# Performance work log

Hardware: AMD Instinct MI355X
Metric: run time of the kernel (lower is better)

Reference implementation:

```python
import jax, jax.numpy as jnp
import numpy as np

B, M, D = 16, 16, 512          # m (tokens per sample) must equal num_experts
N = 16                          # num_experts
H = (D + D) * 2 // 3            # hidden_dim = 682
OUT = 512


def setup_inputs() -> dict:
    key = jax.random.key(0)
    ks = jax.random.split(key, 8)
    s = lambda k, shape, fan: jax.random.normal(k, shape, jnp.float32) / np.sqrt(fan)
    return {
        "x":    jax.random.normal(ks[0], (B, M, D), jnp.float32),
        "phi":  jax.random.normal(ks[1], (D, N, H), jnp.float32),
        "W1":   s(ks[2], (N, D, H), D),
        "b1":   s(ks[3], (N, H), D),
        "W2":   s(ks[4], (N, H, D), H),
        "b2":   s(ks[5], (N, D), H),
        "Wout": s(ks[6], (N * D, OUT), N * D),
        "bout": s(ks[7], (OUT,), N * D),
    }


def reference(x, phi, W1, b1, W2, b2, Wout, bout):
    # dispatch/combine logits: [b, m, n, p]
    logits = jnp.einsum('bmd,dnp->bmnp', x, phi)
    Dw = jax.nn.softmax(logits, axis=1)                       # dispatch weights over tokens m
    Cw = jax.nn.softmax(jax.nn.softmax(logits, axis=2), axis=3)  # (softmax of softmax, faithful)
    Xs = jnp.einsum('bmd,bmnp->bnpd', x, Dw)                  # expert slot inputs [b,n,p,d]
    # batched per-expert MLP (grouped GEMM over expert axis n)
    hmid = jax.nn.relu(jnp.einsum('bnpd,ndh->bnph', Xs, W1) + b1[None, :, None, :])
    Ys = jnp.einsum('bnph,nhd->bnpd', hmid, W2) + b2[None, :, None, :]
    Y = jnp.einsum('bnpd,bmnp->bmd', Ys, Cw)                  # combine -> [b, m, d]
    flat = Y.reshape(Y.shape[0], -1)                          # [b, m*d] == [b, n*d]
    return flat @ Wout + bout
```

## Files before the change

kernel.cpp:

```cpp
#include <hip/hip_runtime.h>
#include <hip/hip_bf16.h>
#include <math.h>

typedef unsigned int   u32;
typedef unsigned short u16;
typedef __bf16 bf16;
typedef bf16  bf16x8  __attribute__((ext_vector_type(8)));
typedef float f32x4   __attribute__((ext_vector_type(4)));
typedef float f32x16  __attribute__((ext_vector_type(16)));

#define BBATCH 16
#define MTOK   16
#define NEXP   16
#define DDIM   512
#define HDIM   682
#define HPAD   704
#define NHCOL  (NEXP*HDIM)
#define NHPCOL (NEXP*HPAD)

__device__ __forceinline__ u16 f2bf(float f) {
    u32 u = __builtin_bit_cast(u32, f);
    u += 0x7fffu + ((u >> 16) & 1u);
    return (u16)(u >> 16);
}
__device__ __forceinline__ float bf2f(u16 h) {
    u32 u = ((u32)h) << 16;
    return __builtin_bit_cast(float, u);
}
__device__ __forceinline__ u32 pk2bf(float a, float b) {
    __hip_bfloat162 t = __float22bfloat162_rn(float2{a, b});
    u32 r;
    __builtin_memcpy(&r, &t, 4);
    return r;
}

__global__ __launch_bounds__(256) void k_prep(
    const float* __restrict__ x, const float* __restrict__ b2,
    const float* __restrict__ bout,
    u16* __restrict__ xh, u16* __restrict__ xl,
    float* __restrict__ Y, float* __restrict__ out, u16* __restrict__ DwT) {
    const int bid = blockIdx.x, tid = threadIdx.x;
    if (bid < 128) {
        int i = (bid * 256 + tid) * 4;
        float4 v = *(const float4*)&x[i];
        float a[4] = {v.x, v.y, v.z, v.w};
        u16 hh[4], ll[4];
        #pragma unroll
        for (int j = 0; j < 4; ++j) {
            hh[j] = f2bf(a[j]);
            ll[j] = f2bf(a[j] - bf2f(hh[j]));
        }
        *(uint2*)&xh[i] = make_uint2((u32)hh[0] | ((u32)hh[1] << 16), (u32)hh[2] | ((u32)hh[3] << 16));
        *(uint2*)&xl[i] = make_uint2((u32)ll[0] | ((u32)ll[1] << 16), (u32)ll[2] | ((u32)ll[3] << 16));
    } else if (bid < 640) {
        int idx = (bid - 128) * 256 + tid;
        int d = idx & 511;
        float s = 0.f;
        #pragma unroll
        for (int nn = 0; nn < 16; ++nn) s += b2[nn * 512 + d];
        Y[idx] = s;
    } else if (bid < 672) {
        int idx = (bid - 640) * 256 + tid;
        out[idx] = bout[idx & 511];
    } else {
        int g = (bid - 672) * 256 + tid;
        int bn = g / 88, off = g - bn * 88;
        *(uint2*)(DwT + (size_t)(bn * HPAD + HDIM) * 16 + off * 4) = make_uint2(0u, 0u);
    }
}

__global__ __launch_bounds__(256) void k_lt1(
    const u16* __restrict__ xh, const u16* __restrict__ xl,
    const float* __restrict__ phi, const float* __restrict__ W1,
    float* __restrict__ logits, u16* __restrict__ DwT, u16* __restrict__ T1b) {
    __shared__ __align__(16) char SMEM[29184];
    const int bid = blockIdx.x, tid = threadIdx.x;
    const int wv = tid >> 6, lane = tid & 63, quad = lane >> 4, l15 = lane & 15;
    if (bid < 684) {
        const int ct = bid % 171, rt = bid / 171;
        u16* AH = (u16*)SMEM;
        u16* AL = (u16*)(SMEM + 5120);
        u16* BH = (u16*)(SMEM + 10240);
        u16* BL = (u16*)(SMEM + 15360);
        float* F = (float*)(SMEM + 20480);
        f32x4 acc[4] = {};
        for (int kb = 0; kb < 512; kb += 32) {
            {
                int r = tid >> 2, kg = (tid & 3) * 8;
                size_t ao = (size_t)(rt * 64 + r) * 512 + kb + kg;
                *(uint4*)&AH[r * 40 + kg] = *(const uint4*)(xh + ao);
                *(uint4*)&AL[r * 40 + kg] = *(const uint4*)(xl + ao);
            }
            {
                int dl = tid >> 3, cg = (tid & 7) * 8;
                int c0 = ct * 64 + cg;
                const float* src = phi + (size_t)(kb + dl) * NHCOL + c0;
                float v[8];
                if (c0 + 8 <= NHCOL) {
                    *(float4*)&v[0] = *(const float4*)&src[0];
                    *(float4*)&v[4] = *(const float4*)&src[4];
                } else {
                    #pragma unroll
                    for (int i = 0; i < 8; ++i) v[i] = (c0 + i < NHCOL) ? src[i] : 0.f;
                }
                #pragma unroll
                for (int i = 0; i < 8; ++i) F[dl * 68 + cg + i] = v[i];
            }
            __syncthreads();
            {
                int cc = tid & 63, q = tid >> 6;
                u16 th[8], tl[8];
                #pragma unroll
                for (int i = 0; i < 8; ++i) {
                    float v = F[(q * 8 + i) * 68 + cc];
                    th[i] = f2bf(v);
                    tl[i] = f2bf(v - bf2f(th[i]));
                }
                *(uint4*)&BH[cc * 40 + q * 8] = *(uint4*)&th[0];
                *(uint4*)&BL[cc * 40 + q * 8] = *(uint4*)&tl[0];
            }
            __syncthreads();
            bf16x8 ah = *(const bf16x8*)&AH[(wv * 16 + l15) * 40 + quad * 8];
            bf16x8 al = *(const bf16x8*)&AL[(wv * 16 + l15) * 40 + quad * 8];
            #pragma unroll
            for (int j = 0; j < 4; ++j) {
                bf16x8 bh = *(const bf16x8*)&BH[(j * 16 + l15) * 40 + quad * 8];
                bf16x8 bl = *(const bf16x8*)&BL[(j * 16 + l15) * 40 + quad * 8];
                acc[j] = __builtin_amdgcn_mfma_f32_16x16x32_bf16(ah, bh, acc[j], 0, 0, 0);
                acc[j] = __builtin_amdgcn_mfma_f32_16x16x32_bf16(ah, bl, acc[j], 0, 0, 0);
                acc[j] = __builtin_amdgcn_mfma_f32_16x16x32_bf16(al, bh, acc[j], 0, 0, 0);
            }
            __syncthreads();
        }
        const int b  = rt * 4 + wv;
        const int r0 = rt * 64 + wv * 16 + quad * 4;
        #pragma unroll
        for (int j = 0; j < 4; ++j) {
            const int col = ct * 64 + j * 16 + l15;
            float a0 = acc[j][0], a1 = acc[j][1], a2 = acc[j][2], a3 = acc[j][3];
            if (col < NHCOL) {
                logits[(size_t)(r0 + 0) * NHCOL + col] = a0;
                logits[(size_t)(r0 + 1) * NHCOL + col] = a1;
                logits[(size_t)(r0 + 2) * NHCOL + col] = a2;
                logits[(size_t)(r0 + 3) * NHCOL + col] = a3;
            }
            float mx = fmaxf(fmaxf(a0, a1), fmaxf(a2, a3));
            mx = fmaxf(mx, __shfl_xor(mx, 16));
            mx = fmaxf(mx, __shfl_xor(mx, 32));
            float e0 = expf(a0 - mx), e1 = expf(a1 - mx);
            float e2 = expf(a2 - mx), e3 = expf(a3 - mx);
            float s = e0 + e1 + e2 + e3;
            s += __shfl_xor(s, 16);
            s += __shfl_xor(s, 32);
            float inv = 1.f / s;
            if (col < NHCOL) {
                int n = col / HDIM;
                int p = col - n * HDIM;
                u16* dst = DwT + ((size_t)((b * 16 + n) * HPAD + p)) * 16 + quad * 4;
                *(uint2*)dst = make_uint2(pk2bf(e0 * inv, e1 * inv), pk2bf(e2 * inv, e3 * inv));
            }
        }
    } else {
        const int w = bid - 684;
        const int ct = w >> 1, rh = w & 1;
        const int n = ct / 11, h0 = (ct % 11) * 64;
        u16* As = (u16*)SMEM;
        u16* Bs = (u16*)(SMEM + 10240);
        float* F = (float*)(SMEM + 15360);
        f32x4 acc[2][4] = {};
        for (int kb = 0; kb < 512; kb += 32) {
            {
                int r = tid >> 1, kg = (tid & 1) * 16;
                const u16* s = xh + (size_t)(rh * 128 + r) * 512 + kb + kg;
                *(uint4*)&As[r * 40 + kg]     = *(const uint4*)s;
                *(uint4*)&As[r * 40 + kg + 8] = *(const uint4*)(s + 8);
            }
            {
                int dl = tid >> 3, cg = (tid & 7) * 8;
                int h = h0 + cg;
                const float* wr = W1 + ((size_t)n * 512 + kb + dl) * HDIM + h;
                float v[8];
                if (h + 8 <= HDIM) {
                    #pragma unroll
                    for (int i = 0; i < 4; ++i) {
                        float2 t = *(const float2*)&wr[i * 2];
                        v[i * 2] = t.x; v[i * 2 + 1] = t.y;
                    }
                } else {
                    #pragma unroll
                    for (int i = 0; i < 8; ++i) v[i] = (h + i < HDIM) ? wr[i] : 0.f;
                }
                #pragma unroll
                for (int i = 0; i < 8; ++i) F[dl * 68 + cg + i] = v[i];
            }
            __syncthreads();
            {
                int cc = tid & 63, q = tid >> 6;
                u16 tv[8];
                #pragma unroll
                for (int i = 0; i < 8; ++i) tv[i] = f2bf(F[(q * 8 + i) * 68 + cc]);
                *(uint4*)&Bs[cc * 40 + q * 8] = *(uint4*)&tv[0];
            }
            __syncthreads();
            bf16x8 af[2], bfr[4];
            #pragma unroll
            for (int i = 0; i < 2; ++i)
                af[i] = *(const bf16x8*)&As[(wv * 32 + i * 16 + l15) * 40 + quad * 8];
            #pragma unroll
            for (int j = 0; j < 4; ++j)
                bfr[j] = *(const bf16x8*)&Bs[(j * 16 + l15) * 40 + quad * 8];
            #pragma unroll
            for (int i = 0; i < 2; ++i)
                #pragma unroll
                for (int j = 0; j < 4; ++j)
                    acc[i][j] = __builtin_amdgcn_mfma_f32_16x16x32_bf16(af[i], bfr[j], acc[i][j], 0, 0, 0);
            __syncthreads();
        }
        #pragma unroll
        for (int i = 0; i < 2; ++i)
            #pragma unroll
            for (int j = 0; j < 4; ++j) {
                int col = ct * 64 + j * 16 + l15;
                int r0  = rh * 128 + wv * 32 + i * 16 + quad * 4;
                #pragma unroll
                for (int r = 0; r < 4; ++r)
                    T1b[(size_t)(r0 + r) * NHPCOL + col] = f2bf(acc[i][j][r]);
            }
    }
}

__global__ __launch_bounds__(256) void k_cw(
    const float* __restrict__ L, u16* __restrict__ CwB) {
    __shared__ float row[NHCOL];
    const int bid = blockIdx.x, tid = threadIdx.x;
    const int m = bid & 15, b = bid >> 4;
    const float* Lrow = L + (size_t)(b * 16 + m) * NHCOL;
    for (int i = tid; i < NHCOL; i += 256) row[i] = Lrow[i];
    __syncthreads();
    for (int p = tid; p < HDIM; p += 256) {
        float v[16];
        float mx = -1e30f;
        #pragma unroll
        for (int n = 0; n < 16; ++n) { v[n] = row[n * HDIM + p]; mx = fmaxf(mx, v[n]); }
        float s = 0.f;
        #pragma unroll
        for (int n = 0; n < 16; ++n) { v[n] = expf(v[n] - mx); s += v[n]; }
        float inv = 1.f / s;
        #pragma unroll
        for (int n = 0; n < 16; ++n) row[n * HDIM + p] = expf(v[n] * inv);
    }
    __syncthreads();
    const int wv = tid >> 6, lane = tid & 63;
    for (int nn = 0; nn < 4; ++nn) {
        int n = wv * 4 + nn;
        float s = 0.f;
        for (int p = lane; p < HDIM; p += 64) s += row[n * HDIM + p];
        #pragma unroll
        for (int off = 32; off > 0; off >>= 1) s += __shfl_xor(s, off);
        float inv = 1.f / s;
        u16* dst = CwB + (size_t)(((b * 16 + n) * 16 + m)) * HPAD;
        for (int p = lane; p < HDIM; p += 64) dst[p] = f2bf(row[n * HDIM + p] * inv);
        if (lane < HPAD - HDIM) dst[HDIM + lane] = 0;
    }
}

__global__ __launch_bounds__(256) void k_mid(
    const u16* __restrict__ T1b, const u16* __restrict__ DwT,
    const u16* __restrict__ CwB, const float* __restrict__ b1,
    u16* __restrict__ Gb) {
    __shared__ u16 T1T[128 * 24];
    __shared__ u16 hmidT[128 * 64];
    const int ht = blockIdx.x, n = blockIdx.y, b = blockIdx.z;
    const int tid = threadIdx.x;
    const int wv = tid >> 6, lane = tid & 63;
    const int quad = lane >> 4, l15 = lane & 15;
    const int l31 = lane & 31, half = lane >> 5;
    const int h0 = ht * 128;
    const int b16n = b * 16 + n;

    {
        int m = tid & 15, hh0 = (tid >> 4) * 8;
        u16 v[8];
        if (h0 + hh0 + 8 <= HPAD) {
            *(uint4*)v = *(const uint4*)(T1b + (size_t)(b * 16 + m) * NHPCOL + n * HPAD + h0 + hh0);
        } else {
            #pragma unroll
            for (int i = 0; i < 8; ++i) v[i] = 0;
        }
        #pragma unroll
        for (int i = 0; i < 8; ++i) T1T[(hh0 + i) * 24 + m] = v[i];
    }
    __syncthreads();

    const int hrow = wv * 32 + l31;
    bf16x8 bt1 = *(const bf16x8*)&T1T[hrow * 24 + half * 8];
    int hg1 = h0 + hrow;
    float biasf = (hg1 < HDIM) ? b1[n * HDIM + hg1] : 0.f;
    f32x16 cbias;
    #pragma unroll
    for (int i = 0; i < 16; ++i) cbias[i] = biasf;

    const u16* dwbase = DwT + (size_t)(b16n * HPAD) * 16;
    const u16* cwrow  = CwB + (size_t)(b16n * 16 + l15) * HPAD;

    f32x4 acc[2] = {};
    const int hsw = hrow & 7;
    for (int c = 0; c < 11; ++c) {
        const int p0 = c * 64;
        #pragma unroll
        for (int pt = 0; pt < 2; ++pt) {
            bf16x8 adw = *(const bf16x8*)(dwbase + (size_t)(p0 + pt * 32 + l31) * 16 + half * 8);
            f32x16 hm = __builtin_amdgcn_mfma_f32_32x32x16_bf16(adw, bt1, cbias, 0, 0, 0);
            #pragma unroll
            for (int g = 0; g < 4; ++g) {
                float v0 = fmaxf(hm[g * 4 + 0], 0.f);
                float v1 = fmaxf(hm[g * 4 + 1], 0.f);
                float v2 = fmaxf(hm[g * 4 + 2], 0.f);
                float v3 = fmaxf(hm[g * 4 + 3], 0.f);
                uint2 pk = make_uint2(pk2bf(v0, v1), pk2bf(v2, v3));
                int gran = (pt * 4 + g) ^ hsw;
                *(uint2*)&hmidT[hrow * 64 + gran * 8 + half * 4] = pk;
            }
        }
        #pragma unroll
        for (int s = 0; s < 2; ++s) {
            bf16x8 acw = *(const bf16x8*)(cwrow + p0 + s * 32 + quad * 8);
            #pragma unroll
            for (int hj = 0; hj < 2; ++hj) {
                int hr = wv * 32 + hj * 16 + l15;
                int gr = (s * 4 + quad) ^ (hr & 7);
                bf16x8 bh = *(const bf16x8*)&hmidT[hr * 64 + gr * 8];
                acc[hj] = __builtin_amdgcn_mfma_f32_16x16x32_bf16(acw, bh, acc[hj], 0, 0, 0);
            }
        }
    }
    #pragma unroll
    for (int hj = 0; hj < 2; ++hj) {
        int h = h0 + wv * 32 + hj * 16 + l15;
        if (h < HPAD) {
            #pragma unroll
            for (int r = 0; r < 4; ++r) {
                int m = quad * 4 + r;
                Gb[(size_t)(b * 16 + m) * NHPCOL + n * HPAD + h] = f2bf(acc[hj][r]);
            }
        }
    }
}

__global__ __launch_bounds__(256) void k_ygemm(
    const u16* __restrict__ G, const float* __restrict__ W2, float* __restrict__ Y) {
    __shared__ u16 AsL[64 * 40];
    __shared__ u16 BsL[128 * 40];
    __shared__ float F[32 * 132];
    const int ct = blockIdx.x, rt = blockIdx.y, nz = blockIdx.z;
    const int n = nz >> 1, kb0 = (nz & 1) * 352;
    const int tid = threadIdx.x;
    const int wv = tid >> 6, lane = tid & 63, quad = lane >> 4, l15 = lane & 15;
    const int m0 = rt * 64, d0 = ct * 128;
    f32x4 acc[4][2] = {};
    for (int kb = kb0; kb < kb0 + 352; kb += 32) {
        {
            int am = tid >> 2, akg = (tid & 3) * 8;
            *(uint4*)&AsL[am * 40 + akg] =
                *(const uint4*)(G + (size_t)(m0 + am) * NHPCOL + n * HPAD + kb + akg);
        }
        {
            int hl = tid >> 3, cg = (tid & 7) * 16;
            int h = kb + hl;
            float v[16];
            if (h < HDIM) {
                const float* src = W2 + ((size_t)n * HDIM + h) * 512 + d0 + cg;
                *(float4*)&v[0]  = *(const float4*)&src[0];
                *(float4*)&v[4]  = *(const float4*)&src[4];
                *(float4*)&v[8]  = *(const float4*)&src[8];
                *(float4*)&v[12] = *(const float4*)&src[12];
            } else {
                #pragma unroll
                for (int i = 0; i < 16; ++i) v[i] = 0.f;
            }
            #pragma unroll
            for (int i = 0; i < 16; ++i) F[hl * 132 + cg + i] = v[i];
        }
        __syncthreads();
        {
            int cc = tid & 127, half = tid >> 7;
            u16 tv[16];
            #pragma unroll
            for (int i = 0; i < 16; ++i) tv[i] = f2bf(F[(half * 16 + i) * 132 + cc]);
            *(uint4*)&BsL[cc * 40 + half * 16]     = *(uint4*)&tv[0];
            *(uint4*)&BsL[cc * 40 + half * 16 + 8] = *(uint4*)&tv[8];
        }
        __syncthreads();
        bf16x8 af[4], bfr[2];
        #pragma unroll
        for (int i = 0; i < 4; ++i) af[i] = *(const bf16x8*)&AsL[(i * 16 + l15) * 40 + quad * 8];
        #pragma unroll
        for (int j = 0; j < 2; ++j) bfr[j] = *(const bf16x8*)&BsL[(wv * 32 + j * 16 + l15) * 40 + quad * 8];
        #pragma unroll
        for (int i = 0; i < 4; ++i)
            #pragma unroll
            for (int j = 0; j < 2; ++j)
                acc[i][j] = __builtin_amdgcn_mfma_f32_16x16x32_bf16(af[i], bfr[j], acc[i][j], 0, 0, 0);
        __syncthreads();
    }
    #pragma unroll
    for (int i = 0; i < 4; ++i)
        #pragma unroll
        for (int j = 0; j < 2; ++j) {
            int d = d0 + wv * 32 + j * 16 + l15;
            int r0 = m0 + i * 16 + quad * 4;
            #pragma unroll
            for (int r = 0; r < 4; ++r)
                atomicAdd(&Y[(size_t)(r0 + r) * 512 + d], acc[i][j][r]);
        }
}

__global__ __launch_bounds__(256) void k_outgemm(
    const float* __restrict__ Y, const float* __restrict__ Wout, float* __restrict__ out) {
    __shared__ u16 AsL[16 * 40];
    __shared__ u16 BsL[128 * 40];
    __shared__ float F[32 * 132];
    const int ct = blockIdx.x, ks = blockIdx.y;
    const int tid = threadIdx.x;
    const int wv = tid >> 6, lane = tid & 63, quad = lane >> 4, l15 = lane & 15;
    const int o0 = ct * 128, kbase = ks * 64;
    f32x4 acc[2] = {};
    for (int kb = 0; kb < 64; kb += 32) {
        {
            int r = tid >> 4, k2 = (tid & 15) * 2;
            float2 v = *(const float2*)&Y[(size_t)r * 8192 + kbase + kb + k2];
            AsL[r * 40 + k2]     = f2bf(v.x);
            AsL[r * 40 + k2 + 1] = f2bf(v.y);
        }
        {
            int kl = tid >> 3, cg = (tid & 7) * 16;
            const float* src = Wout + (size_t)(kbase + kb + kl) * 512 + o0 + cg;
            float v[16];
            *(float4*)&v[0]  = *(const float4*)&src[0];
            *(float4*)&v[4]  = *(const float4*)&src[4];
            *(float4*)&v[8]  = *(const float4*)&src[8];
            *(float4*)&v[12] = *(const float4*)&src[12];
            #pragma unroll
            for (int i = 0; i < 16; ++i) F[kl * 132 + cg + i] = v[i];
        }
        __syncthreads();
        {
            int cc = tid & 127, half = tid >> 7;
            u16 tv[16];
            #pragma unroll
            for (int i = 0; i < 16; ++i) tv[i] = f2bf(F[(half * 16 + i) * 132 + cc]);
            *(uint4*)&BsL[cc * 40 + half * 16]     = *(uint4*)&tv[0];
            *(uint4*)&BsL[cc * 40 + half * 16 + 8] = *(uint4*)&tv[8];
        }
        __syncthreads();
        bf16x8 af = *(const bf16x8*)&AsL[l15 * 40 + quad * 8];
        #pragma unroll
        for (int j = 0; j < 2; ++j) {
            bf16x8 bfr = *(const bf16x8*)&BsL[(wv * 32 + j * 16 + l15) * 40 + quad * 8];
            acc[j] = __builtin_amdgcn_mfma_f32_16x16x32_bf16(af, bfr, acc[j], 0, 0, 0);
        }
        __syncthreads();
    }
    #pragma unroll
    for (int j = 0; j < 2; ++j) {
        int o = o0 + wv * 32 + j * 16 + l15;
        #pragma unroll
        for (int r = 0; r < 4; ++r)
            atomicAdd(&out[(size_t)(quad * 4 + r) * 512 + o], acc[j][r]);
    }
}

extern "C" void kernel_launch(void* const* d_in, const int* in_sizes, int n_in,
                              void* d_out, int out_size, void* d_ws, size_t ws_size,
                              hipStream_t stream) {
    const float* x    = (const float*)d_in[0];
    const float* phi  = (const float*)d_in[1];
    const float* W1   = (const float*)d_in[2];
    const float* b1   = (const float*)d_in[3];
    const float* W2   = (const float*)d_in[4];
    const float* b2   = (const float*)d_in[5];
    const float* Wout = (const float*)d_in[6];
    const float* bout = (const float*)d_in[7];
    float* out = (float*)d_out;

    char* base = (char*)d_ws;
    float* logits = (float*)(base + 0);
    u16*   DwT    = (u16*)(base + 11173888);
    u16*   CwB    = (u16*)(base + 16941056);
    u16*   T1b    = (u16*)(base + 22708224);
    u16*   Gb     = (u16*)(base + 28475392);
    u16*   xh     = (u16*)(base + 34242560);
    u16*   xl     = (u16*)(base + 34504704);
    float* Y      = (float*)(base + 34766848);

    k_prep    <<<dim3(760), 256, 0, stream>>>(x, b2, bout, xh, xl, Y, out, DwT);
    k_lt1     <<<dim3(1036), 256, 0, stream>>>(xh, xl, phi, W1, logits, DwT, T1b);
    k_cw      <<<dim3(256), 256, 0, stream>>>(logits, CwB);
    k_mid     <<<dim3(6, 16, 16), 256, 0, stream>>>(T1b, DwT, CwB, b1, Gb);
    k_ygemm   <<<dim3(4, 4, 32), 256, 0, stream>>>(Gb, W2, Y);
    k_outgemm <<<dim3(4, 128), 256, 0, stream>>>(Y, Wout, out);
}
```

Measured before the change: 226.0 us.

## Prefetch next K-tile into registers and remap blocks for XCD-aware L2 reuse

In the logits, W1 and W2 GEMM kernels, the next K-step's global loads now go into registers before the MFMA work on the current tile, so memory latency overlaps compute. Block indices are remapped so that blocks sharing the same weight columns or expert land on the same XCD (bid & 7), which should improve L2 reuse of phi, W1 and W2. The k_lt1 grid is padded to 704 logits blocks, with early return for unused tiles. The prefetch raises register pressure, which may lower occupancy.

```diff
diff --git a/kernel.cpp b/kernel.cpp
--- a/kernel.cpp
+++ b/kernel.cpp
@@ -76,37 +76,46 @@
     __shared__ __align__(16) char SMEM[29184];
     const int bid = blockIdx.x, tid = threadIdx.x;
     const int wv = tid >> 6, lane = tid & 63, quad = lane >> 4, l15 = lane & 15;
-    if (bid < 684) {
-        const int ct = bid % 171, rt = bid / 171;
+    if (bid < 704) {
+        const int xcd = bid & 7, slot = bid >> 3;
+        const int rt = slot & 3, ct = (slot >> 2) * 8 + xcd;
+        if (ct >= 171) return;
         u16* AH = (u16*)SMEM;
         u16* AL = (u16*)(SMEM + 5120);
         u16* BH = (u16*)(SMEM + 10240);
         u16* BL = (u16*)(SMEM + 15360);
         float* F = (float*)(SMEM + 20480);
+        const int r = tid >> 2, kg = (tid & 3) * 8;
+        const u16* aph = xh + (size_t)(rt * 64 + r) * 512 + kg;
+        const u16* apl = xl + (size_t)(rt * 64 + r) * 512 + kg;
+        const int dl = tid >> 3, cg = (tid & 7) * 8;
+        const int c0 = ct * 64 + cg;
+        float vB[8];
+        auto loadB = [&](int kb) {
+            const float* src = phi + (size_t)(kb + dl) * NHCOL + c0;
+            if (c0 + 8 <= NHCOL) {
+                *(float4*)&vB[0] = *(const float4*)&src[0];
+                *(float4*)&vB[4] = *(const float4*)&src[4];
+            } else {
+                #pragma unroll
+                for (int i = 0; i < 8; ++i) vB[i] = (c0 + i < NHCOL) ? src[i] : 0.f;
+            }
+        };
+        uint4 rAh = *(const uint4*)aph;
+        uint4 rAl = *(const uint4*)apl;
+        loadB(0);
         f32x4 acc[4] = {};
         for (int kb = 0; kb < 512; kb += 32) {
-            {
-                int r = tid >> 2, kg = (tid & 3) * 8;
-                size_t ao = (size_t)(rt * 64 + r) * 512 + kb + kg;
-                *(uint4*)&AH[r * 40 + kg] = *(const uint4*)(xh + ao);
-                *(uint4*)&AL[r * 40 + kg] = *(const uint4*)(xl + ao);
-            }
-            {
-                int dl = tid >> 3, cg = (tid & 7) * 8;
-                int c0 = ct * 64 + cg;
-                const float* src = phi + (size_t)(kb + dl) * NHCOL + c0;
-                float v[8];
-                if (c0 + 8 <= NHCOL) {
-                    *(float4*)&v[0] = *(const float4*)&src[0];
-                    *(float4*)&v[4] = *(const float4*)&src[4];
-                } else {
-                    #pragma unroll
-                    for (int i = 0; i < 8; ++i) v[i] = (c0 + i < NHCOL) ? src[i] : 0.f;
-                }
-                #pragma unroll
-                for (int i = 0; i < 8; ++i) F[dl * 68 + cg + i] = v[i];
-            }
+            *(uint4*)&AH[r * 40 + kg] = rAh;
+            *(uint4*)&AL[r * 40 + kg] = rAl;
+            *(float4*)&F[dl * 68 + cg]     = *(float4*)&vB[0];
+            *(float4*)&F[dl * 68 + cg + 4] = *(float4*)&vB[4];
             __syncthreads();
+            if (kb + 32 < 512) {
+                rAh = *(const uint4*)(aph + kb + 32);
+                rAl = *(const uint4*)(apl + kb + 32);
+                loadB(kb + 32);
+            }
             {
                 int cc = tid & 63, q = tid >> 6;
                 u16 th[8], tl[8];
@@ -161,39 +170,46 @@
             }
         }
     } else {
-        const int w = bid - 684;
-        const int ct = w >> 1, rh = w & 1;
+        const int b2_ = bid - 704;
+        const int xcd = b2_ & 7, slot = b2_ >> 3;
+        const int rh = slot & 1, ct = (slot >> 1) * 8 + xcd;
         const int n = ct / 11, h0 = (ct % 11) * 64;
         u16* As = (u16*)SMEM;
         u16* Bs = (u16*)(SMEM + 10240);
         float* F = (float*)(SMEM + 15360);
+        const int r = tid >> 1, kg = (tid & 1) * 16;
+        const u16* ap = xh + (size_t)(rh * 128 + r) * 512 + kg;
+        const int dl = tid >> 3, cg = (tid & 7) * 8;
+        const int h = h0 + cg;
+        float vB[8];
+        auto loadB = [&](int kb) {
+            const float* wr = W1 + ((size_t)n * 512 + kb + dl) * HDIM + h;
+            if (h + 8 <= HDIM) {
+                #pragma unroll
+                for (int i = 0; i < 4; ++i) {
+                    float2 t = *(const float2*)&wr[i * 2];
+                    vB[i * 2] = t.x; vB[i * 2 + 1] = t.y;
+                }
+            } else {
+                #pragma unroll
+                for (int i = 0; i < 8; ++i) vB[i] = (h + i < HDIM) ? wr[i] : 0.f;
+            }
+        };
+        uint4 rA0 = *(const uint4*)ap;
+        uint4 rA1 = *(const uint4*)(ap + 8);
+        loadB(0);
         f32x4 acc[2][4] = {};
         for (int kb = 0; kb < 512; kb += 32) {
-            {
-                int r = tid >> 1, kg = (tid & 1) * 16;
-                const u16* s = xh + (size_t)(rh * 128 + r) * 512 + kb + kg;
-                *(uint4*)&As[r * 40 + kg]     = *(const uint4*)s;
-                *(uint4*)&As[r * 40 + kg + 8] = *(const uint4*)(s + 8);
-            }
-            {
-                int dl = tid >> 3, cg = (tid & 7) * 8;
-                int h = h0 + cg;
-                const float* wr = W1 + ((size_t)n * 512 + kb + dl) * HDIM + h;
-                float v[8];
-                if (h + 8 <= HDIM) {
-                    #pragma unroll
-                    for (int i = 0; i < 4; ++i) {
-                        float2 t = *(const float2*)&wr[i * 2];
-                        v[i * 2] = t.x; v[i * 2 + 1] = t.y;
-                    }
-                } else {
-                    #pragma unroll
-                    for (int i = 0; i < 8; ++i) v[i] = (h + i < HDIM) ? wr[i] : 0.f;
-                }
-                #pragma unroll
-                for (int i = 0; i < 8; ++i) F[dl * 68 + cg + i] = v[i];
-            }
+            *(uint4*)&As[r * 40 + kg]     = rA0;
+            *(uint4*)&As[r * 40 + kg + 8] = rA1;
+            *(float4*)&F[dl * 68 + cg]     = *(float4*)&vB[0];
+            *(float4*)&F[dl * 68 + cg + 4] = *(float4*)&vB[4];
             __syncthreads();
+            if (kb + 32 < 512) {
+                rA0 = *(const uint4*)(ap + kb + 32);
+                rA1 = *(const uint4*)(ap + kb + 40);
+                loadB(kb + 32);
+            }
             {
                 int cc = tid & 63, q = tid >> 6;
                 u16 tv[8];
@@ -223,8 +239,8 @@
                 int col = ct * 64 + j * 16 + l15;
                 int r0  = rh * 128 + wv * 32 + i * 16 + quad * 4;
                 #pragma unroll
-                for (int r = 0; r < 4; ++r)
-                    T1b[(size_t)(r0 + r) * NHPCOL + col] = f2bf(acc[i][j][r]);
+                for (int rr = 0; rr < 4; ++rr)
+                    T1b[(size_t)(r0 + rr) * NHPCOL + col] = f2bf(acc[i][j][rr]);
             }
     }
 }
@@ -270,7 +286,11 @@
     u16* __restrict__ Gb) {
     __shared__ u16 T1T[128 * 24];
     __shared__ u16 hmidT[128 * 64];
-    const int ht = blockIdx.x, n = blockIdx.y, b = blockIdx.z;
+    const int bid = blockIdx.x;
+    const int xcd = bid & 7, slot = bid >> 3;
+    const int ht = slot % 6, gg = slot / 6;
+    const int g = gg * 8 + xcd;
+    const int n = g & 15, b = g >> 4;
     const int tid = threadIdx.x;
     const int wv = tid >> 6, lane = tid & 63;
     const int quad = lane >> 4, l15 = lane & 15;
@@ -312,13 +332,13 @@
             bf16x8 adw = *(const bf16x8*)(dwbase + (size_t)(p0 + pt * 32 + l31) * 16 + half * 8);
             f32x16 hm = __builtin_amdgcn_mfma_f32_32x32x16_bf16(adw, bt1, cbias, 0, 0, 0);
             #pragma unroll
-            for (int g = 0; g < 4; ++g) {
-                float v0 = fmaxf(hm[g * 4 + 0], 0.f);
-                float v1 = fmaxf(hm[g * 4 + 1], 0.f);
-                float v2 = fmaxf(hm[g * 4 + 2], 0.f);
-                float v3 = fmaxf(hm[g * 4 + 3], 0.f);
+            for (int g2 = 0; g2 < 4; ++g2) {
+                float v0 = fmaxf(hm[g2 * 4 + 0], 0.f);
+                float v1 = fmaxf(hm[g2 * 4 + 1], 0.f);
+                float v2 = fmaxf(hm[g2 * 4 + 2], 0.f);
+                float v3 = fmaxf(hm[g2 * 4 + 3], 0.f);
                 uint2 pk = make_uint2(pk2bf(v0, v1), pk2bf(v2, v3));
-                int gran = (pt * 4 + g) ^ hsw;
+                int gran = (pt * 4 + g2) ^ hsw;
                 *(uint2*)&hmidT[hrow * 64 + gran * 8 + half * 4] = pk;
             }
         }
@@ -352,36 +372,46 @@
     __shared__ u16 AsL[64 * 40];
     __shared__ u16 BsL[128 * 40];
     __shared__ float F[32 * 132];
-    const int ct = blockIdx.x, rt = blockIdx.y, nz = blockIdx.z;
+    const int bid = blockIdx.x;
+    const int xcd = bid & 7, slot = bid >> 3;
+    const int rt = slot & 3, gg = slot >> 2;
+    const int g = gg * 8 + xcd;
+    const int ct = g & 3, nz = g >> 2;
     const int n = nz >> 1, kb0 = (nz & 1) * 352;
     const int tid = threadIdx.x;
     const int wv = tid >> 6, lane = tid & 63, quad = lane >> 4, l15 = lane & 15;
     const int m0 = rt * 64, d0 = ct * 128;
+    const int am = tid >> 2, akg = (tid & 3) * 8;
+    const u16* apg = G + (size_t)(m0 + am) * NHPCOL + n * HPAD + akg;
+    const int hl = tid >> 3, cg = (tid & 7) * 16;
+    float vB[16];
+    auto loadB = [&](int kb) {
+        int h = kb + hl;
+        if (h < HDIM) {
+            const float* src = W2 + ((size_t)n * HDIM + h) * 512 + d0 + cg;
+            *(float4*)&vB[0]  = *(const float4*)&src[0];
+            *(float4*)&vB[4]  = *(const float4*)&src[4];
+            *(float4*)&vB[8]  = *(const float4*)&src[8];
+            *(float4*)&vB[12] = *(const float4*)&src[12];
+        } else {
+            #pragma unroll
+            for (int i = 0; i < 16; ++i) vB[i] = 0.f;
+        }
+    };
+    uint4 rA = *(const uint4*)(apg + kb0);
+    loadB(kb0);
     f32x4 acc[4][2] = {};
     for (int kb = kb0; kb < kb0 + 352; kb += 32) {
-        {
-            int am = tid >> 2, akg = (tid & 3) * 8;
-            *(uint4*)&AsL[am * 40 + akg] =
-                *(const uint4*)(G + (size_t)(m0 + am) * NHPCOL + n * HPAD + kb + akg);
-        }
-        {
-            int hl = tid >> 3, cg = (tid & 7) * 16;
-            int h = kb + hl;
-            float v[16];
-            if (h < HDIM) {
-                const float* src = W2 + ((size_t)n * HDIM + h) * 512 + d0 + cg;
-                *(float4*)&v[0]  = *(const float4*)&src[0];
-                *(float4*)&v[4]  = *(const float4*)&src[4];
-                *(float4*)&v[8]  = *(const float4*)&src[8];
-                *(float4*)&v[12] = *(const float4*)&src[12];
-            } else {
-                #pragma unroll
-                for (int i = 0; i < 16; ++i) v[i] = 0.f;
-            }
-            #pragma unroll
-            for (int i = 0; i < 16; ++i) F[hl * 132 + cg + i] = v[i];
-        }
+        *(uint4*)&AsL[am * 40 + akg] = rA;
+        *(float4*)&F[hl * 132 + cg]      = *(float4*)&vB[0];
+        *(float4*)&F[hl * 132 + cg + 4]  = *(float4*)&vB[4];
+        *(float4*)&F[hl * 132 + cg + 8]  = *(float4*)&vB[8];
+        *(float4*)&F[hl * 132 + cg + 12] = *(float4*)&vB[12];
         __syncthreads();
+        if (kb + 32 < kb0 + 352) {
+            rA = *(const uint4*)(apg + kb + 32);
+            loadB(kb + 32);
+        }
         {
             int cc = tid & 127, half = tid >> 7;
             u16 tv[16];
@@ -494,9 +524,9 @@
     float* Y      = (float*)(base + 34766848);
 
     k_prep    <<<dim3(760), 256, 0, stream>>>(x, b2, bout, xh, xl, Y, out, DwT);
-    k_lt1     <<<dim3(1036), 256, 0, stream>>>(xh, xl, phi, W1, logits, DwT, T1b);
+    k_lt1     <<<dim3(1056), 256, 0, stream>>>(xh, xl, phi, W1, logits, DwT, T1b);
     k_cw      <<<dim3(256), 256, 0, stream>>>(logits, CwB);
-    k_mid     <<<dim3(6, 16, 16), 256, 0, stream>>>(T1b, DwT, CwB, b1, Gb);
-    k_ygemm   <<<dim3(4, 4, 32), 256, 0, stream>>>(Gb, W2, Y);
+    k_mid     <<<dim3(1536), 256, 0, stream>>>(T1b, DwT, CwB, b1, Gb);
+    k_ygemm   <<<dim3(512), 256, 0, stream>>>(Gb, W2, Y);
     k_outgemm <<<dim3(4, 128), 256, 0, stream>>>(Y, Wout, out);
 }
```

Measured after the change: 216.3 us. 1.05x faster.
